# Optimization experiments

Measured on AMD Instinct MI355X. Metric: run time of the kernel, lower is better.

Reference implementation:

```python
import jax, jax.numpy as jnp
import numpy as np

B, L, E, MODES = 32, 1024, 512, 64


def setup_inputs() -> dict:
    key = jax.random.key(0)
    k1, k2, k3 = jax.random.split(key, 3)
    scale = 1.0 / (E * E)
    q = jax.random.normal(k1, (B, L, E), dtype=jnp.float32)
    # torch.rand(..., dtype=cfloat) -> real and imag each uniform [0,1)
    w_real = scale * jax.random.uniform(k2, (E, E, MODES), dtype=jnp.float32)
    w_imag = scale * jax.random.uniform(k3, (E, E, MODES), dtype=jnp.float32)
    return {"q": q, "w_real": w_real, "w_imag": w_imag}


def reference(q, w_real, w_imag):
    # mode_select_method='lowest': index = [0..MODES-1], sorted
    index = jnp.arange(MODES)
    x = jnp.transpose(q, (0, 2, 1))            # [B, E, L]
    x_ft = jnp.fft.rfft(x, axis=-1)            # [B, E, L//2+1] complex
    xg = x_ft[:, :, index]                     # gather selected modes [B, E, M]
    W = w_real + 1j * w_imag                   # [E_in, E_out, M] complex
    # fused batched complex GEMM over all modes (replaces per-mode loop)
    out_modes = jnp.einsum('bhm,him->bim', xg, W)  # [B, E, M]
    F = L // 2 + 1
    out_ft = jnp.zeros((B, E, F), dtype=out_modes.dtype)
    # original writes results at positions wi = 0..M-1 (loop index), not at `index`
    out_ft = out_ft.at[:, :, :MODES].set(out_modes)
    x_out = jnp.fft.irfft(out_ft, n=L, axis=-1)    # [B, E, L] real
    return jnp.transpose(x_out, (0, 2, 1))         # [B, L, E]
```

## Files before the change

kernel.cpp:

```cpp
#include <hip/hip_runtime.h>
#include <math.h>

#define LQ 1024
#define EQ 512
#define BQ 32
#define MQ 64

static constexpr int BCHUNK = LQ * EQ;

typedef short short8 __attribute__((ext_vector_type(8)));
typedef float f32x4 __attribute__((ext_vector_type(4)));
typedef unsigned short ushort_t;

union FragI { int i[4]; int4 v; short8 s; };

__device__ inline char* sx_ptr(float* dout, int arr, int m, int b, int h) {
    unsigned G = ((unsigned)arr << 20) + ((unsigned)m << 14) +
                 ((unsigned)(h >> 5) << 10) + ((unsigned)b << 5) + (unsigned)(h & 31);
    unsigned z = G >> 19, w = G & 524287u;
    return (char*)(dout + (size_t)z * BCHUNK + 262144) + (size_t)w * 2;
}

__device__ inline void split2(float a, float b, unsigned& hi, unsigned& lo) {
    unsigned ua = __float_as_uint(a), ub = __float_as_uint(b);
    unsigned ha = ua & 0xFFFF0000u, hb = ub & 0xFFFF0000u;
    hi = (ua >> 16) | hb;
    float la = a - __uint_as_float(ha);
    float lb = b - __uint_as_float(hb);
    lo = (__float_as_uint(la) >> 16) | (__float_as_uint(lb) & 0xFFFF0000u);
}

__device__ inline void split1(float x, ushort_t& hi, ushort_t& lo) {
    unsigned u = __float_as_uint(x);
    hi = (ushort_t)(u >> 16);
    float r = x - __uint_as_float(u & 0xFFFF0000u);
    lo = (ushort_t)(__float_as_uint(r) >> 16);
}

__global__ __launch_bounds__(256) void k_trig(unsigned* __restrict__ BFhi,
                                              unsigned* __restrict__ BFlo,
                                              float* __restrict__ dout) {
    int idx = blockIdx.x * 256 + threadIdx.x;
    int l = idx >> 6, m = idx & 63;
    int tt = (l * m) & (LQ - 1);
    float ang = (float)tt * 6.135923151542565e-03f;
    float s, c;
    sincosf(ang, &s, &c);
    float coef = (m == 0 ? 1.0f : 2.0f) * (1.0f / (float)LQ);
    float b0 = coef * c;
    float b1 = (m == 0) ? 0.0f : (-2.0f / (float)LQ) * s;
    unsigned hi, lo;
    split2(b0, b1, hi, lo);
    {
        int lt = l >> 4, kb = m >> 4, kgb = (m & 15) >> 2;
        int lane = kgb * 16 + (l & 15);
        int u = lt * 1024 + kb * 256 + lane * 4 + (m & 3);
        BFhi[u] = hi;
        BFlo[u] = lo;
    }
    ushort_t* THs = (ushort_t*)dout;
    ushort_t* TLs = (ushort_t*)(dout + 65536);
    int ks = l >> 5, kg = (l >> 3) & 3, j = l & 7;
    int mt = m >> 3;
    int lane0 = kg * 16 + 2 * (m & 7);
    ushort_t ch, cl, sh, sl;
    split1(c, ch, cl);
    split1(-s, sh, sl);
    int u0 = ((ks * 8 + mt) * 64 + lane0) * 8 + j;
    THs[u0] = ch;  TLs[u0] = cl;
    THs[u0 + 8] = sh;  TLs[u0 + 8] = sl;
}

__global__ __launch_bounds__(512) void k_dft3(const float* __restrict__ q,
                                              float* __restrict__ dout) {
    __shared__ float qs[64][34];
    const int t    = threadIdx.x;
    const int wave = t >> 6;
    const int lane = t & 63;
    const int a    = wave & 3;
    const int ht   = wave >> 2;
    const int b    = blockIdx.x >> 4;
    const int hg   = blockIdx.x & 15;
    const int hbase = hg * 32;
    const int col  = lane & 15;
    const int kg   = lane >> 4;
    const float* qb = q + (size_t)b * BCHUNK;
    const int4* TH4 = (const int4*)dout;
    const int4* TL4 = (const int4*)(dout + 65536);

    f32x4 acc[2] = {{0.f, 0.f, 0.f, 0.f}, {0.f, 0.f, 0.f, 0.f}};
    float2 st2[2];
#define LOADQ(CC)                                                             \
    {                                                                         \
        int l0_ = (CC) * 64;                                                  \
        _Pragma("unroll")                                                     \
        for (int r = 0; r < 2; ++r) {                                         \
            int e = r * 512 + t;                                              \
            int lp = e >> 4, hc = (e & 15) * 2;                               \
            st2[r] = *(const float2*)&qb[(size_t)(l0_ + lp) * EQ + hbase + hc]; \
        }                                                                     \
    }

    LOADQ(0);
#define MM(A, B, C) C = __builtin_amdgcn_mfma_f32_16x16x32_bf16(A, B, C, 0, 0, 0)
    for (int cchunk = 0; cchunk < 16; ++cchunk) {
#pragma unroll
        for (int r = 0; r < 2; ++r) {
            int e = r * 512 + t;
            int lp = e >> 4, hc = (e & 15) * 2;
            *(float2*)&qs[lp][hc] = st2[r];
        }
        __syncthreads();
        if (cchunk < 15) LOADQ(cchunk + 1);
#pragma unroll
        for (int ksl = 0; ksl < 2; ++ksl) {
            const int ks = cchunk * 2 + ksl;
            float v[8];
#pragma unroll
            for (int j = 0; j < 8; ++j)
                v[j] = qs[ksl * 32 + kg * 8 + j][ht * 16 + col];
            FragI bhiF, bloF;
#pragma unroll
            for (int k = 0; k < 4; ++k) {
                unsigned h_, l_;
                split2(v[2 * k], v[2 * k + 1], h_, l_);
                bhiF.i[k] = (int)h_;
                bloF.i[k] = (int)l_;
            }
#pragma unroll
            for (int ti = 0; ti < 2; ++ti) {
                int mt = 2 * a + ti;
                FragI ah, al;
                ah.v = TH4[(ks * 8 + mt) * 64 + lane];
                al.v = TL4[(ks * 8 + mt) * 64 + lane];
                MM(ah.s, bhiF.s, acc[ti]);
                MM(ah.s, bloF.s, acc[ti]);
                MM(al.s, bhiF.s, acc[ti]);
            }
        }
        __syncthreads();
    }
#undef MM
#undef LOADQ
    const int h = hbase + ht * 16 + col;
#pragma unroll
    for (int ti = 0; ti < 2; ++ti) {
        int mt = 2 * a + ti;
        int mA = mt * 8 + kg * 2;
#pragma unroll
        for (int mi = 0; mi < 2; ++mi) {
            float xr = acc[ti][2 * mi];
            float xi = acc[ti][2 * mi + 1];
            ushort_t rh, rl, ih_, il_;
            split1(xr, rh, rl);
            split1(xi, ih_, il_);
            int m = mA + mi;
            *(ushort_t*)sx_ptr(dout, 0, m, b, h) = rh;
            *(ushort_t*)sx_ptr(dout, 1, m, b, h) = rl;
            *(ushort_t*)sx_ptr(dout, 2, m, b, h) = ih_;
            *(ushort_t*)sx_ptr(dout, 3, m, b, h) = il_;
            *(ushort_t*)sx_ptr(dout, 4, m, b, h) = (ushort_t)(ih_ ^ 0x8000);
            *(ushort_t*)sx_ptr(dout, 5, m, b, h) = (ushort_t)(il_ ^ 0x8000);
        }
    }
}

__global__ __launch_bounds__(512) void k_modes5(const float* __restrict__ wreal,
                                                const float* __restrict__ wimag,
                                                float* __restrict__ dout) {
    __shared__ float Wlds[2 * 32 * 16 * 18];
    const int t    = threadIdx.x;
    const int wave = t >> 6;
    const int lane = t & 63;
    const int blk  = blockIdx.x;
    const int hs   = blk >> 7;
    const int mc   = (blk >> 5) & 3;
    const int it   = blk & 31;
    const int i0   = it * 16;
    const int m0   = mc * 16;
    const int col  = lane & 15;
    const int kg   = lane >> 4;
    const int hbase = hs * 128;

    const char* xp0 = sx_ptr(dout, 0, m0 + 2 * wave, col, hbase + kg * 8);

    f32x4 zero4 = {0.f, 0.f, 0.f, 0.f};
    f32x4 acc[2][2][2];
#pragma unroll
    for (int a = 0; a < 2; ++a)
#pragma unroll
        for (int bq = 0; bq < 2; ++bq)
#pragma unroll
            for (int c = 0; c < 2; ++c) acc[a][bq][c] = zero4;

    float2 st[16];
#define LOADK(KK)                                                             \
    {                                                                         \
        int h0_ = hbase + (KK) * 32;                                          \
        _Pragma("unroll")                                                     \
        for (int r = 0; r < 16; ++r) {                                        \
            int e = r * 512 + t;                                              \
            int m2 = e & 7, ii = (e >> 3) & 15, hh = (e >> 7) & 31;           \
            const float* src = (e >> 12) ? wimag : wreal;                     \
            st[r] = *(const float2*)&src[(size_t)(h0_ + hh) * 32768 +         \
                                         (size_t)(i0 + ii) * 64 + m0 + 2 * m2]; \
        }                                                                     \
    }

    LOADK(0);
    for (int kk = 0; kk < 4; ++kk) {
#pragma unroll
        for (int r = 0; r < 16; ++r) {
            int e = r * 512 + t;
            int m2 = e & 7, ii = (e >> 3) & 15, hh = (e >> 7) & 31;
            int part = e >> 12;
            *(float2*)&Wlds[(((part * 32 + hh) * 16) + ii) * 18 + 2 * m2] = st[r];
        }
        __syncthreads();
        if (kk < 3) LOADK(kk + 1);
#pragma unroll
        for (int mi = 0; mi < 2; ++mi) {
            const int mloc = 2 * wave + mi;
            short8 aW[2][2];
#pragma unroll
            for (int part = 0; part < 2; ++part) {
                float v[8];
#pragma unroll
                for (int j = 0; j < 8; ++j)
                    v[j] = Wlds[((part * 32 + kg * 8 + j) * 16 + col) * 18 + mloc];
                FragI hiF, loF;
#pragma unroll
                for (int k = 0; k < 4; ++k) {
                    unsigned h, l;
                    split2(v[2 * k], v[2 * k + 1], h, l);
                    hiF.i[k] = (int)h;
                    loF.i[k] = (int)l;
                }
                aW[part][0] = hiF.s;
                aW[part][1] = loF.s;
            }
            const char* xpm = xp0 + (size_t)mi * 32768 + (size_t)kk * 2048;
#define MM(A, B, C) C = __builtin_amdgcn_mfma_f32_16x16x32_bf16(A, B, C, 0, 0, 0)
#pragma unroll
            for (int nt = 0; nt < 2; ++nt) {
                short8 bX[6];
#pragma unroll
                for (int arr = 0; arr < 6; ++arr) {
                    FragI f;
                    f.v = *(const int4*)(xpm + (size_t)arr * 4194304 +
                                         (size_t)nt * 1024);
                    bX[arr] = f.s;
                }
                MM(aW[0][0], bX[0], acc[mi][0][nt]);
                MM(aW[0][0], bX[1], acc[mi][0][nt]);
                MM(aW[0][1], bX[0], acc[mi][0][nt]);
                MM(aW[1][0], bX[4], acc[mi][0][nt]);
                MM(aW[1][0], bX[5], acc[mi][0][nt]);
                MM(aW[1][1], bX[4], acc[mi][0][nt]);
                MM(aW[0][0], bX[2], acc[mi][1][nt]);
                MM(aW[0][0], bX[3], acc[mi][1][nt]);
                MM(aW[0][1], bX[2], acc[mi][1][nt]);
                MM(aW[1][0], bX[0], acc[mi][1][nt]);
                MM(aW[1][0], bX[1], acc[mi][1][nt]);
                MM(aW[1][1], bX[0], acc[mi][1][nt]);
            }
#undef MM
        }
        __syncthreads();
    }
#undef LOADK
#pragma unroll
    for (int mi = 0; mi < 2; ++mi)
#pragma unroll
        for (int part = 0; part < 2; ++part)
#pragma unroll
            for (int nt = 0; nt < 2; ++nt) {
                int bb = nt * 16 + col;
                int c = 2 * (m0 + 2 * wave + mi) + part;
                f32x4 vv = acc[mi][part][nt];
                float4 o = make_float4(vv.x, vv.y, vv.z, vv.w);
                *(float4*)&dout[(size_t)bb * BCHUNK + (size_t)hs * 65536 +
                                (size_t)c * EQ + i0 + kg * 4] = o;
            }
}

__global__ __launch_bounds__(256) void k_inv3(const unsigned* __restrict__ BFhi,
                                              const unsigned* __restrict__ BFlo,
                                              float* __restrict__ dout) {
    __shared__ unsigned Bf[4096];
    const int t    = threadIdx.x;
    const int wave = t >> 6;
    const int lane = t & 63;
    const int b    = blockIdx.x >> 4;
    const int it   = blockIdx.x & 15;
    const int i0   = it * 32;
    float* base = dout + (size_t)b * BCHUNK;

#pragma unroll
    for (int r = 0; r < 8; ++r) {
        int idx = r * 256 + t;
        int il = idx & 31, cp = idx >> 5;
        int c0 = 2 * cp;
        const float* p0 = base + (size_t)c0 * EQ + i0 + il;
        float s0 = p0[0] + p0[65536] + p0[2 * 65536] + p0[3 * 65536];
        const float* p1 = p0 + EQ;
        float s1 = p1[0] + p1[65536] + p1[2 * 65536] + p1[3 * 65536];
        unsigned hi, lo;
        split2(s0, s1, hi, lo);
        int nt = il >> 4, i_loc = il & 15;
        int kb = c0 >> 5, kg = (c0 & 31) >> 3, jp = (c0 & 7) >> 1;
        int u = (nt * 4 + kb) * 256 + (kg * 16 + i_loc) * 4 + jp;
        Bf[u] = hi;
        Bf[2048 + u] = lo;
    }
    __syncthreads();
    FragI bh[2][4], bl[2][4];
#pragma unroll
    for (int nt = 0; nt < 2; ++nt)
#pragma unroll
        for (int kb = 0; kb < 4; ++kb) {
            bh[nt][kb].v = *(const int4*)&Bf[(nt * 4 + kb) * 256 + lane * 4];
            bl[nt][kb].v = *(const int4*)&Bf[2048 + (nt * 4 + kb) * 256 + lane * 4];
        }
#define MM(A, B, C) C = __builtin_amdgcn_mfma_f32_16x16x32_bf16(A, B, C, 0, 0, 0)
    for (int r = 0; r < 16; ++r) {
        int lt = wave + 4 * r;
        FragI ah[4], al[4];
#pragma unroll
        for (int kb = 0; kb < 4; ++kb) {
            ah[kb].v = *(const int4*)&BFhi[lt * 1024 + kb * 256 + lane * 4];
            al[kb].v = *(const int4*)&BFlo[lt * 1024 + kb * 256 + lane * 4];
        }
        f32x4 a0 = {0.f, 0.f, 0.f, 0.f}, a1 = {0.f, 0.f, 0.f, 0.f};
#pragma unroll
        for (int kb = 0; kb < 4; ++kb) {
            MM(ah[kb].s, bh[0][kb].s, a0);
            MM(ah[kb].s, bl[0][kb].s, a0);
            MM(al[kb].s, bh[0][kb].s, a0);
            MM(ah[kb].s, bh[1][kb].s, a1);
            MM(ah[kb].s, bl[1][kb].s, a1);
            MM(al[kb].s, bh[1][kb].s, a1);
        }
        int lrow = lt * 16 + (lane >> 4) * 4;
        int icol = i0 + (lane & 15);
#pragma unroll
        for (int j = 0; j < 4; ++j) {
            base[(size_t)(lrow + j) * EQ + icol]      = a0[j];
            base[(size_t)(lrow + j) * EQ + icol + 16] = a1[j];
        }
    }
#undef MM
}

extern "C" void kernel_launch(void* const* d_in, const int* in_sizes, int n_in,
                              void* d_out, int out_size, void* d_ws, size_t ws_size,
                              hipStream_t stream) {
    const float* q  = (const float*)d_in[0];
    const float* wr = (const float*)d_in[1];
    const float* wi = (const float*)d_in[2];
    float* out = (float*)d_out;
    unsigned* BFhi = (unsigned*)d_ws;
    unsigned* BFlo = BFhi + 65536;

    hipLaunchKernelGGL(k_trig,   dim3(256), dim3(256), 0, stream, BFhi, BFlo, out);
    hipLaunchKernelGGL(k_dft3,   dim3(512), dim3(512), 0, stream, q, out);
    hipLaunchKernelGGL(k_modes5, dim3(512), dim3(512), 0, stream, wr, wi, out);
    hipLaunchKernelGGL(k_inv3,   dim3(512), dim3(256), 0, stream, BFhi, BFlo, out);
}
```

Measured before the change: 135.9 us.

## Use direct global-to-LDS loads and software pipelining in DFT and mode GEMM kernels

Both the forward DFT kernel and the mode-mixing kernel now load their tiles with global_load_lds, which writes to shared memory without staging through registers. The DFT kernel gets a double-buffered LDS tile, drops its second barrier and prefetches the twiddle fragments. The mode kernel uses an XOR-swizzled LDS layout and interleaves X fragment loads with the MFMA groups. It also stops storing the negated imaginary arrays and flips the sign bits of the weight fragments in registers instead. This removes register staging, one barrier per step and two output arrays, but the direct LDS path and the occupancy hint of 4 blocks per CU put more pressure on registers and make the synchronisation more delicate.

```diff
diff --git a/kernel.cpp b/kernel.cpp
--- a/kernel.cpp
+++ b/kernel.cpp
@@ -13,6 +13,12 @@
 typedef unsigned short ushort_t;
 
 union FragI { int i[4]; int4 v; short8 s; };
+
+__device__ __forceinline__ void gload16(const float* g, float* l) {
+    __builtin_amdgcn_global_load_lds(
+        (const __attribute__((address_space(1))) void*)g,
+        (__attribute__((address_space(3))) void*)l, 16, 0, 0);
+}
 
 __device__ inline char* sx_ptr(float* dout, int arr, int m, int b, int h) {
     unsigned G = ((unsigned)arr << 20) + ((unsigned)m << 14) +
@@ -71,9 +77,11 @@
     THs[u0 + 8] = sh;  TLs[u0 + 8] = sl;
 }
 
-__global__ __launch_bounds__(512) void k_dft3(const float* __restrict__ q,
-                                              float* __restrict__ dout) {
-    __shared__ float qs[64][34];
+#define MM(A, B, C) C = __builtin_amdgcn_mfma_f32_16x16x32_bf16(A, B, C, 0, 0, 0)
+
+__global__ __launch_bounds__(512, 4) void k_dft4(const float* __restrict__ q,
+                                                 float* __restrict__ dout) {
+    __shared__ float qs[2 * 2048];
     const int t    = threadIdx.x;
     const int wave = t >> 6;
     const int lane = t & 63;
@@ -89,59 +97,49 @@
     const int4* TL4 = (const int4*)(dout + 65536);
 
     f32x4 acc[2] = {{0.f, 0.f, 0.f, 0.f}, {0.f, 0.f, 0.f, 0.f}};
-    float2 st2[2];
-#define LOADQ(CC)                                                             \
-    {                                                                         \
-        int l0_ = (CC) * 64;                                                  \
-        _Pragma("unroll")                                                     \
-        for (int r = 0; r < 2; ++r) {                                         \
-            int e = r * 512 + t;                                              \
-            int lp = e >> 4, hc = (e & 15) * 2;                               \
-            st2[r] = *(const float2*)&qb[(size_t)(l0_ + lp) * EQ + hbase + hc]; \
-        }                                                                     \
-    }
-
-    LOADQ(0);
-#define MM(A, B, C) C = __builtin_amdgcn_mfma_f32_16x16x32_bf16(A, B, C, 0, 0, 0)
-    for (int cchunk = 0; cchunk < 16; ++cchunk) {
-#pragma unroll
-        for (int r = 0; r < 2; ++r) {
-            int e = r * 512 + t;
-            int lp = e >> 4, hc = (e & 15) * 2;
-            *(float2*)&qs[lp][hc] = st2[r];
-        }
+    const int lp = wave * 8 + (lane >> 3);
+    const int hq = 4 * (lane & 7);
+
+    gload16(qb + (size_t)lp * EQ + hbase + hq, &qs[wave * 256]);
+
+    int cur = 0;
+    for (int cc = 0; cc < 16; ++cc) {
         __syncthreads();
-        if (cchunk < 15) LOADQ(cchunk + 1);
+        FragI ah[2][2], al[2][2];
+#pragma unroll
+        for (int ksl = 0; ksl < 2; ++ksl)
+#pragma unroll
+            for (int ti = 0; ti < 2; ++ti) {
+                int idx = ((cc * 2 + ksl) * 8 + 2 * a + ti) * 64 + lane;
+                ah[ksl][ti].v = TH4[idx];
+                al[ksl][ti].v = TL4[idx];
+            }
+        if (cc < 15)
+            gload16(qb + (size_t)((cc + 1) * 64 + lp) * EQ + hbase + hq,
+                    &qs[(cur ^ 1) * 2048 + wave * 256]);
 #pragma unroll
         for (int ksl = 0; ksl < 2; ++ksl) {
-            const int ks = cchunk * 2 + ksl;
             float v[8];
 #pragma unroll
             for (int j = 0; j < 8; ++j)
-                v[j] = qs[ksl * 32 + kg * 8 + j][ht * 16 + col];
+                v[j] = qs[cur * 2048 + (ksl * 32 + kg * 8 + j) * 32 + ht * 16 + col];
             FragI bhiF, bloF;
 #pragma unroll
-            for (int k = 0; k < 4; ++k) {
+            for (int k2 = 0; k2 < 4; ++k2) {
                 unsigned h_, l_;
-                split2(v[2 * k], v[2 * k + 1], h_, l_);
-                bhiF.i[k] = (int)h_;
-                bloF.i[k] = (int)l_;
+                split2(v[2 * k2], v[2 * k2 + 1], h_, l_);
+                bhiF.i[k2] = (int)h_;
+                bloF.i[k2] = (int)l_;
             }
 #pragma unroll
             for (int ti = 0; ti < 2; ++ti) {
-                int mt = 2 * a + ti;
-                FragI ah, al;
-                ah.v = TH4[(ks * 8 + mt) * 64 + lane];
-                al.v = TL4[(ks * 8 + mt) * 64 + lane];
-                MM(ah.s, bhiF.s, acc[ti]);
-                MM(ah.s, bloF.s, acc[ti]);
-                MM(al.s, bhiF.s, acc[ti]);
+                MM(ah[ksl][ti].s, bhiF.s, acc[ti]);
+                MM(ah[ksl][ti].s, bloF.s, acc[ti]);
+                MM(al[ksl][ti].s, bhiF.s, acc[ti]);
             }
         }
-        __syncthreads();
-    }
-#undef MM
-#undef LOADQ
+        cur ^= 1;
+    }
     const int h = hbase + ht * 16 + col;
 #pragma unroll
     for (int ti = 0; ti < 2; ++ti) {
@@ -159,16 +157,14 @@
             *(ushort_t*)sx_ptr(dout, 1, m, b, h) = rl;
             *(ushort_t*)sx_ptr(dout, 2, m, b, h) = ih_;
             *(ushort_t*)sx_ptr(dout, 3, m, b, h) = il_;
-            *(ushort_t*)sx_ptr(dout, 4, m, b, h) = (ushort_t)(ih_ ^ 0x8000);
-            *(ushort_t*)sx_ptr(dout, 5, m, b, h) = (ushort_t)(il_ ^ 0x8000);
-        }
-    }
-}
-
-__global__ __launch_bounds__(512) void k_modes5(const float* __restrict__ wreal,
-                                                const float* __restrict__ wimag,
-                                                float* __restrict__ dout) {
-    __shared__ float Wlds[2 * 32 * 16 * 18];
+        }
+    }
+}
+
+__global__ __launch_bounds__(512, 4) void k_modes7(const float* __restrict__ wreal,
+                                                   const float* __restrict__ wimag,
+                                                   float* __restrict__ dout) {
+    __shared__ float Wlds[16384];
     const int t    = threadIdx.x;
     const int wave = t >> 6;
     const int lane = t & 63;
@@ -193,82 +189,98 @@
 #pragma unroll
             for (int c = 0; c < 2; ++c) acc[a][bq][c] = zero4;
 
-    float2 st[16];
-#define LOADK(KK)                                                             \
+    FragI xA[4], xB[4];
+    short8 aW[2][2];
+    short8 nW[2];
+
+#define LDX(BUF, MI, NT, KK)                                                  \
     {                                                                         \
-        int h0_ = hbase + (KK) * 32;                                          \
+        const char* xpm_ = xp0 + (size_t)(MI) * 32768 +                       \
+                           (size_t)(KK) * 2048 + (size_t)(NT) * 1024;         \
+        BUF[0].v = *(const int4*)(xpm_);                                      \
+        BUF[1].v = *(const int4*)(xpm_ + 4194304);                            \
+        BUF[2].v = *(const int4*)(xpm_ + 2 * 4194304);                        \
+        BUF[3].v = *(const int4*)(xpm_ + 3 * 4194304);                        \
+    }
+
+#define READW(MI)                                                             \
+    {                                                                         \
+        const int mloc_ = 2 * wave + (MI);                                    \
+        const int mb4_ = mloc_ >> 2;                                          \
+        const int mo_ = mloc_ & 3;                                            \
         _Pragma("unroll")                                                     \
-        for (int r = 0; r < 16; ++r) {                                        \
-            int e = r * 512 + t;                                              \
-            int m2 = e & 7, ii = (e >> 3) & 15, hh = (e >> 7) & 31;           \
-            const float* src = (e >> 12) ? wimag : wreal;                     \
-            st[r] = *(const float2*)&src[(size_t)(h0_ + hh) * 32768 +         \
-                                         (size_t)(i0 + ii) * 64 + m0 + 2 * m2]; \
+        for (int part = 0; part < 2; ++part) {                                \
+            float v[8];                                                       \
+            _Pragma("unroll")                                                 \
+            for (int j = 0; j < 8; ++j)                                       \
+                v[j] = Wlds[part * 8192 + (kg * 8 + j) * 256 + col * 16 +     \
+                            ((mb4_ ^ kg) << 2) + mo_];                        \
+            FragI hiF, loF;                                                   \
+            _Pragma("unroll")                                                 \
+            for (int k2 = 0; k2 < 4; ++k2) {                                  \
+                unsigned h_, l_;                                              \
+                split2(v[2 * k2], v[2 * k2 + 1], h_, l_);                     \
+                hiF.i[k2] = (int)h_;                                          \
+                loF.i[k2] = (int)l_;                                          \
+            }                                                                 \
+            aW[part][0] = hiF.s;                                              \
+            aW[part][1] = loF.s;                                              \
         }                                                                     \
-    }
-
-    LOADK(0);
+        FragI th_, tl_, nh_, nl_;                                             \
+        th_.s = aW[1][0]; tl_.s = aW[1][1];                                   \
+        _Pragma("unroll")                                                     \
+        for (int k2 = 0; k2 < 4; ++k2) {                                      \
+            nh_.i[k2] = th_.i[k2] ^ 0x80008000;                               \
+            nl_.i[k2] = tl_.i[k2] ^ 0x80008000;                               \
+        }                                                                     \
+        nW[0] = nh_.s;                                                        \
+        nW[1] = nl_.s;                                                        \
+    }
+
+#define MMG(MI, NT, BUF)                                                      \
+    MM(aW[0][0], BUF[0].s, acc[MI][0][NT]);                                   \
+    MM(aW[0][0], BUF[1].s, acc[MI][0][NT]);                                   \
+    MM(aW[0][1], BUF[0].s, acc[MI][0][NT]);                                   \
+    MM(nW[0],    BUF[2].s, acc[MI][0][NT]);                                   \
+    MM(nW[0],    BUF[3].s, acc[MI][0][NT]);                                   \
+    MM(nW[1],    BUF[2].s, acc[MI][0][NT]);                                   \
+    MM(aW[0][0], BUF[2].s, acc[MI][1][NT]);                                   \
+    MM(aW[0][0], BUF[3].s, acc[MI][1][NT]);                                   \
+    MM(aW[0][1], BUF[2].s, acc[MI][1][NT]);                                   \
+    MM(aW[1][0], BUF[0].s, acc[MI][1][NT]);                                   \
+    MM(aW[1][0], BUF[1].s, acc[MI][1][NT]);                                   \
+    MM(aW[1][1], BUF[0].s, acc[MI][1][NT]);
+
+    LDX(xA, 0, 0, 0);
     for (int kk = 0; kk < 4; ++kk) {
-#pragma unroll
-        for (int r = 0; r < 16; ++r) {
-            int e = r * 512 + t;
-            int m2 = e & 7, ii = (e >> 3) & 15, hh = (e >> 7) & 31;
-            int part = e >> 12;
-            *(float2*)&Wlds[(((part * 32 + hh) * 16) + ii) * 18 + 2 * m2] = st[r];
-        }
         __syncthreads();
-        if (kk < 3) LOADK(kk + 1);
-#pragma unroll
-        for (int mi = 0; mi < 2; ++mi) {
-            const int mloc = 2 * wave + mi;
-            short8 aW[2][2];
-#pragma unroll
-            for (int part = 0; part < 2; ++part) {
-                float v[8];
-#pragma unroll
-                for (int j = 0; j < 8; ++j)
-                    v[j] = Wlds[((part * 32 + kg * 8 + j) * 16 + col) * 18 + mloc];
-                FragI hiF, loF;
-#pragma unroll
-                for (int k = 0; k < 4; ++k) {
-                    unsigned h, l;
-                    split2(v[2 * k], v[2 * k + 1], h, l);
-                    hiF.i[k] = (int)h;
-                    loF.i[k] = (int)l;
-                }
-                aW[part][0] = hiF.s;
-                aW[part][1] = loF.s;
-            }
-            const char* xpm = xp0 + (size_t)mi * 32768 + (size_t)kk * 2048;
-#define MM(A, B, C) C = __builtin_amdgcn_mfma_f32_16x16x32_bf16(A, B, C, 0, 0, 0)
-#pragma unroll
-            for (int nt = 0; nt < 2; ++nt) {
-                short8 bX[6];
-#pragma unroll
-                for (int arr = 0; arr < 6; ++arr) {
-                    FragI f;
-                    f.v = *(const int4*)(xpm + (size_t)arr * 4194304 +
-                                         (size_t)nt * 1024);
-                    bX[arr] = f.s;
-                }
-                MM(aW[0][0], bX[0], acc[mi][0][nt]);
-                MM(aW[0][0], bX[1], acc[mi][0][nt]);
-                MM(aW[0][1], bX[0], acc[mi][0][nt]);
-                MM(aW[1][0], bX[4], acc[mi][0][nt]);
-                MM(aW[1][0], bX[5], acc[mi][0][nt]);
-                MM(aW[1][1], bX[4], acc[mi][0][nt]);
-                MM(aW[0][0], bX[2], acc[mi][1][nt]);
-                MM(aW[0][0], bX[3], acc[mi][1][nt]);
-                MM(aW[0][1], bX[2], acc[mi][1][nt]);
-                MM(aW[1][0], bX[0], acc[mi][1][nt]);
-                MM(aW[1][0], bX[1], acc[mi][1][nt]);
-                MM(aW[1][1], bX[0], acc[mi][1][nt]);
-            }
-#undef MM
+#pragma unroll
+        for (int r = 0; r < 8; ++r) {
+            const int W64 = r * 8 + wave;
+            const int part = W64 >> 5;
+            const int h = W64 & 31;
+            const int hx = (h >> 3) & 3;
+            const float* srcb = part ? wimag : wreal;
+            const float* src = srcb +
+                (size_t)(hbase + kk * 32 + h) * 32768 +
+                (size_t)(i0 + (lane >> 2)) * 64 + m0 + 4 * ((lane & 3) ^ hx);
+            gload16(src, &Wlds[W64 * 256]);
         }
         __syncthreads();
-    }
-#undef LOADK
+        LDX(xB, 0, 1, kk);
+        READW(0);
+        MMG(0, 0, xA);
+        LDX(xA, 1, 0, kk);
+        MMG(0, 1, xB);
+        READW(1);
+        LDX(xB, 1, 1, kk);
+        MMG(1, 0, xA);
+        if (kk < 3) LDX(xA, 0, 0, kk + 1);
+        MMG(1, 1, xB);
+    }
+#undef LDX
+#undef READW
+#undef MMG
 #pragma unroll
     for (int mi = 0; mi < 2; ++mi)
 #pragma unroll
@@ -322,7 +334,6 @@
             bh[nt][kb].v = *(const int4*)&Bf[(nt * 4 + kb) * 256 + lane * 4];
             bl[nt][kb].v = *(const int4*)&Bf[2048 + (nt * 4 + kb) * 256 + lane * 4];
         }
-#define MM(A, B, C) C = __builtin_amdgcn_mfma_f32_16x16x32_bf16(A, B, C, 0, 0, 0)
     for (int r = 0; r < 16; ++r) {
         int lt = wave + 4 * r;
         FragI ah[4], al[4];
@@ -349,8 +360,8 @@
             base[(size_t)(lrow + j) * EQ + icol + 16] = a1[j];
         }
     }
+}
 #undef MM
-}
 
 extern "C" void kernel_launch(void* const* d_in, const int* in_sizes, int n_in,
                               void* d_out, int out_size, void* d_ws, size_t ws_size,
@@ -363,7 +374,7 @@
     unsigned* BFlo = BFhi + 65536;
 
     hipLaunchKernelGGL(k_trig,   dim3(256), dim3(256), 0, stream, BFhi, BFlo, out);
-    hipLaunchKernelGGL(k_dft3,   dim3(512), dim3(512), 0, stream, q, out);
-    hipLaunchKernelGGL(k_modes5, dim3(512), dim3(512), 0, stream, wr, wi, out);
+    hipLaunchKernelGGL(k_dft4,   dim3(512), dim3(512), 0, stream, q, out);
+    hipLaunchKernelGGL(k_modes7, dim3(512), dim3(512), 0, stream, wr, wi, out);
     hipLaunchKernelGGL(k_inv3,   dim3(512), dim3(256), 0, stream, BFhi, BFlo, out);
 }
```

New measurement: 143.4 us. 5.5% more time.
